# Kernel tuning notes

Hardware: AMD Instinct MI355X
Metric: run time of the kernel (lower is better)

Reference implementation:

```python
import jax, jax.numpy as jnp
import numpy as np

B, NPG, C, DEG, DE = 64, 1024, 512, 32, 16  # graphs, nodes/graph, feat dim, avg degree, edge-feat dim
N = B * NPG
E = N * DEG
RATIO = 0.5


def setup_inputs() -> dict:
    key = jax.random.key(0)
    k1, k2, k3, k4 = jax.random.split(key, 4)
    x = jax.random.normal(k1, (N, C), dtype=jnp.float32)
    # edges drawn within each graph block so batch structure is respected
    local = jax.random.randint(k2, (2, E), 0, NPG, dtype=jnp.int32)
    offsets = jnp.repeat(jnp.arange(B, dtype=jnp.int32) * NPG, NPG * DEG)
    edge_index = local + offsets[None, :]
    edge_attr = jax.random.normal(k3, (E, DE), dtype=jnp.float32)
    batch = jnp.repeat(jnp.arange(B, dtype=jnp.int32), NPG)
    W = jax.random.normal(k4, (C, 1), dtype=jnp.float32) * (1.0 / np.sqrt(C))
    b = jnp.zeros((1,), dtype=jnp.float32)
    return {"x": x, "edge_index": edge_index, "edge_attr": edge_attr, "batch": batch,
            "W": W, "b": b, "num_graphs": B, "nodes_per_graph": NPG}


def _gcn_score(x, edge_index, W, b):
    # PyG GCNConv(in_channels, 1): add self-loops, symmetric D^-1/2 (A+I) D^-1/2 norm
    n = x.shape[0]
    loop = jnp.arange(n, dtype=edge_index.dtype)
    s = jnp.concatenate([edge_index[0], loop])
    d = jnp.concatenate([edge_index[1], loop])
    deg = jnp.zeros((n,), x.dtype).at[d].add(jnp.ones((), x.dtype))  # >= 1 via self loops
    dinv = jax.lax.rsqrt(deg)
    norm = dinv[s] * dinv[d]                       # [E+n]
    h = (x @ W)[:, 0]                               # project first: [n]
    score = jnp.zeros((n,), x.dtype).at[d].add(h[s] * norm) + b[0]
    return score


def reference(x, edge_index, edge_attr, batch, W, b, num_graphs, nodes_per_graph):
    n = x.shape[0]
    k = int(np.ceil(RATIO * nodes_per_graph))
    score = _gcn_score(x, edge_index, W, b)         # [n]
    # per-graph top-k (equal-sized graphs -> fixed-shape top_k over [B, NPG])
    sc = score.reshape(num_graphs, nodes_per_graph)
    _, topi = jax.lax.top_k(sc, k)                  # [B, k], score-descending per graph
    offs = (jnp.arange(num_graphs, dtype=edge_index.dtype) * nodes_per_graph)[:, None]
    perm = (topi.astype(edge_index.dtype) + offs).reshape(-1)  # [B*k]
    x_new = x[perm] * jnp.tanh(score[perm])[:, None]
    batch_new = batch[perm]
    # filter_adj: keep edges with both endpoints selected, remap to new ids.
    # Fixed-shape version: full-length edge list with invalid entries = -1 plus a mask.
    sel = jnp.zeros((n,), bool).at[perm].set(True)
    newidx = jnp.full((n,), -1, edge_index.dtype).at[perm].set(
        jnp.arange(perm.shape[0], dtype=edge_index.dtype))
    src, dst = edge_index[0], edge_index[1]
    edge_mask = sel[src] & sel[dst]                 # [E]
    ei_new = jnp.where(edge_mask[None, :], jnp.stack([newidx[src], newidx[dst]]), -1)
    ea_new = jnp.where(edge_mask[:, None], edge_attr, jnp.zeros((), edge_attr.dtype))
    return x_new, ei_new, ea_new, edge_mask, batch_new, perm
```

## Files before the change

kernel.cpp:

```cpp
#include <hip/hip_runtime.h>
#include <math.h>

#define N_NODES 65536
#define C_DIM   512
#define E_EDGES 2097152
#define DE_DIM  16
#define B_GR    64
#define NPG     1024
#define DEG     32
#define EPG     (NPG * DEG)
#define K_SEL   512
#define NK      (B_GR * K_SEL)

#define OUT_XNEW  0
#define OUT_EI    (NK * C_DIM)
#define OUT_EA    (OUT_EI + 2 * E_EDGES)
#define OUT_MASK  (OUT_EA + (size_t)E_EDGES * DE_DIM)
#define OUT_BATCH (OUT_MASK + E_EDGES)
#define OUT_PERM  (OUT_BATCH + NK)

#define HIST_BLKS B_GR

__global__ void k_front(const float* __restrict__ x,
                        const float* __restrict__ W,
                        const int* __restrict__ dst,
                        float* __restrict__ h,
                        float* __restrict__ di) {
    __shared__ int   cnt[NPG];
    __shared__ float sW[C_DIM];

    if (blockIdx.x < HIST_BLKS) {
        const int g = blockIdx.x, t = threadIdx.x;
#pragma unroll
        for (int i = 0; i < 4; ++i) cnt[t + 256 * i] = 0;
        __syncthreads();

        const int4* dv = (const int4*)(dst + (size_t)g * EPG);
#pragma unroll
        for (int i = 0; i < 32; ++i) {
            int4 a = dv[t + 256 * i];
            atomicAdd(&cnt[a.x & (NPG - 1)], 1);
            atomicAdd(&cnt[a.y & (NPG - 1)], 1);
            atomicAdd(&cnt[a.z & (NPG - 1)], 1);
            atomicAdd(&cnt[a.w & (NPG - 1)], 1);
        }
        __syncthreads();

#pragma unroll
        for (int i = 0; i < 4; ++i) {
            const int n = t + 256 * i;
            di[(size_t)g * NPG + n] = rsqrtf((float)cnt[n] + 1.0f);
        }
    } else {
        const int t = threadIdx.x;
        ((float2*)sW)[t] = ((const float2*)W)[t];
        __syncthreads();

        const int wave = t >> 6, lane = t & 63;
        const int node = (blockIdx.x - HIST_BLKS) * 4 + wave;
        const float* xr = x + (size_t)node * C_DIM + lane * 8;
        float4 a0 = ((const float4*)xr)[0];
        float4 a1 = ((const float4*)xr)[1];
        const float* wr = sW + lane * 8;
        float s = a0.x * wr[0] + a0.y * wr[1] + a0.z * wr[2] + a0.w * wr[3]
                + a1.x * wr[4] + a1.y * wr[5] + a1.z * wr[6] + a1.w * wr[7];
#pragma unroll
        for (int off = 32; off > 0; off >>= 1) s += __shfl_down(s, off, 64);
        if (lane == 0) h[node] = s;
    }
}

__global__ void __launch_bounds__(1024)
k_select(const int* __restrict__ src, const int* __restrict__ dst,
         const float* __restrict__ h, const float* __restrict__ di,
         const float* __restrict__ b,
         int*   __restrict__ newidx, int* __restrict__ permw,
         float* __restrict__ mult,
         float* __restrict__ out_perm, float* __restrict__ out_batch) {
    __shared__ float hd[NPG];
    __shared__ float scp[NPG];
    __shared__ float scs[NPG];
    __shared__ unsigned long long keys[NPG];

    const int g = blockIdx.x, t = threadIdx.x;
    const int nbase = g * NPG;

    const float di_t = di[nbase + t];
    hd[t]  = h[nbase + t] * di_t;
    scp[t] = 0.0f;
    __syncthreads();

    const int4* sv = (const int4*)(src + (size_t)g * EPG);
    const int4* dv = (const int4*)(dst + (size_t)g * EPG);
#pragma unroll
    for (int i = 0; i < 8; ++i) {
        int4 sa = sv[t + NPG * i];
        int4 da = dv[t + NPG * i];
        unsafeAtomicAdd(&scp[da.x & (NPG - 1)], hd[sa.x & (NPG - 1)]);
        unsafeAtomicAdd(&scp[da.y & (NPG - 1)], hd[sa.y & (NPG - 1)]);
        unsafeAtomicAdd(&scp[da.z & (NPG - 1)], hd[sa.z & (NPG - 1)]);
        unsafeAtomicAdd(&scp[da.w & (NPG - 1)], hd[sa.w & (NPG - 1)]);
    }
    __syncthreads();

    {
        const float scf = (scp[t] + hd[t]) * di_t + b[0];
        scs[t] = scf;
        const unsigned int bits = __float_as_uint(scf);
        const unsigned int u = bits ^ ((bits & 0x80000000u) ? 0xFFFFFFFFu : 0x80000000u);
        keys[t] = ((unsigned long long)(~u) << 32) | (unsigned int)t;
    }
    __syncthreads();

    for (int k = 2; k <= NPG; k <<= 1) {
        for (int j = k >> 1; j > 0; j >>= 1) {
            if (t < NPG / 2) {
                const int i = ((t & ~(j - 1)) << 1) | (t & (j - 1));
                const int p = i | j;
                const bool asc = (i & k) == 0;
                const unsigned long long a = keys[i], bb = keys[p];
                if ((a > bb) == asc) { keys[i] = bb; keys[p] = a; }
            }
            __syncthreads();
        }
    }

    const int li   = (int)(keys[t] & 0xFFFFFFFFull);
    const int node = nbase + li;
    if (t < K_SEL) {
        const int j  = g * K_SEL + t;
        permw[j]     = node;
        newidx[node] = j;
        mult[j]      = tanhf(scs[li]);
        out_perm[j]  = (float)node;
        out_batch[j] = (float)g;
    } else {
        newidx[node] = -1;
    }
}

#define EDGE_BLKS (E_EDGES / 64)
#define XNEW_BLKS (NK / 2)

__global__ void k_tail(const float* __restrict__ x,
                       const float* __restrict__ mult,
                       const int* __restrict__ permw,
                       const int* __restrict__ src,
                       const int* __restrict__ dst,
                       const float* __restrict__ ea,
                       const int* __restrict__ newidx,
                       float* __restrict__ out_xnew,
                       float* __restrict__ out_ei,
                       float* __restrict__ out_ea,
                       float* __restrict__ out_mask) {
    int bid = blockIdx.x;
    if (bid < EDGE_BLKS) {
        const int gid = bid * 256 + threadIdx.x;
        const int e = gid >> 2, c = gid & 3;
        const int s = src[e], d = dst[e];
        const int ns = newidx[s], nd = newidx[d];
        const bool m = (ns >= 0) && (nd >= 0);

        float4 v = make_float4(0.f, 0.f, 0.f, 0.f);
        if (m) v = ((const float4*)ea)[(size_t)e * 4 + c];
        ((float4*)out_ea)[(size_t)e * 4 + c] = v;

        if (c == 0) {
            out_ei[e]           = m ? (float)ns : -1.0f;
            out_ei[E_EDGES + e] = m ? (float)nd : -1.0f;
            out_mask[e]         = m ? 1.0f : 0.0f;
        }
    } else {
        bid -= EDGE_BLKS;
        const int row = bid * 2 + (threadIdx.x >> 7);
        const int c   = (threadIdx.x & 127) * 4;
        const int node = permw[row];
        const float tt = mult[row];
        float4 v = *(const float4*)(x + (size_t)node * C_DIM + c);
        v.x *= tt; v.y *= tt; v.z *= tt; v.w *= tt;
        *(float4*)(out_xnew + (size_t)row * C_DIM + c) = v;
    }
}

extern "C" void kernel_launch(void* const* d_in, const int* in_sizes, int n_in,
                              void* d_out, int out_size, void* d_ws, size_t ws_size,
                              hipStream_t stream) {
    const float* x  = (const float*)d_in[0];
    const int*   ei = (const int*)d_in[1];
    const float* ea = (const float*)d_in[2];
    const float* W  = (const float*)d_in[4];
    const float* b  = (const float*)d_in[5];
    const int* src = ei;
    const int* dst = ei + E_EDGES;

    float* out = (float*)d_out;

    float* h      = (float*)d_ws;
    float* di     = h + N_NODES;
    float* mult   = di + N_NODES;
    int*   permw  = (int*)(mult + NK);
    int*   newidx = permw + NK;

    k_front<<<HIST_BLKS + N_NODES / 4, 256, 0, stream>>>(x, W, dst, h, di);
    k_select<<<B_GR, 1024, 0, stream>>>(src, dst, h, di, b,
                                        newidx, permw, mult,
                                        out + OUT_PERM, out + OUT_BATCH);
    k_tail<<<EDGE_BLKS + XNEW_BLKS, 256, 0, stream>>>(x, mult, permw, src, dst, ea,
                                                      newidx, out + OUT_XNEW,
                                                      out + OUT_EI, out + OUT_EA,
                                                      out + OUT_MASK);
}
```

Measured before the change: 481.6 us.

## Split score scatter across blocks, register bitonic sort, nontemporal tail accesses

The per-graph edge scatter moves into a separate kernel that splits each graph's edges over four blocks and merges partial sums with global atomics, so 256 blocks run instead of 64. Top-k becomes a register-resident bitonic sort that uses wave shuffles for strides below 64 and shared memory only for larger strides, which halves idle threads and cuts barriers. The streaming loads and stores in the tail kernel become nontemporal to avoid polluting the cache. The cost is an extra launch, global float atomics that make the summation order nondeterministic, and a score buffer that has to be zeroed.

```diff
diff --git a/kernel.cpp b/kernel.cpp
--- a/kernel.cpp
+++ b/kernel.cpp
@@ -9,8 +9,12 @@
 #define NPG     1024
 #define DEG     32
 #define EPG     (NPG * DEG)
+#define PARTS   4
+#define EPP     (EPG / PARTS)
 #define K_SEL   512
 #define NK      (B_GR * K_SEL)
+
+typedef float f32x4 __attribute__((ext_vector_type(4)));
 
 #define OUT_XNEW  0
 #define OUT_EI    (NK * C_DIM)
@@ -25,7 +29,8 @@
                         const float* __restrict__ W,
                         const int* __restrict__ dst,
                         float* __restrict__ h,
-                        float* __restrict__ di) {
+                        float* __restrict__ di,
+                        float* __restrict__ score) {
     __shared__ int   cnt[NPG];
     __shared__ float sW[C_DIM];
 
@@ -49,7 +54,8 @@
 #pragma unroll
         for (int i = 0; i < 4; ++i) {
             const int n = t + 256 * i;
-            di[(size_t)g * NPG + n] = rsqrtf((float)cnt[n] + 1.0f);
+            di[(size_t)g * NPG + n]    = rsqrtf((float)cnt[n] + 1.0f);
+            score[(size_t)g * NPG + n] = 0.0f;
         }
     } else {
         const int t = threadIdx.x;
@@ -71,61 +77,79 @@
 }
 
 __global__ void __launch_bounds__(1024)
-k_select(const int* __restrict__ src, const int* __restrict__ dst,
-         const float* __restrict__ h, const float* __restrict__ di,
-         const float* __restrict__ b,
-         int*   __restrict__ newidx, int* __restrict__ permw,
-         float* __restrict__ mult,
-         float* __restrict__ out_perm, float* __restrict__ out_batch) {
+k_score(const int* __restrict__ src, const int* __restrict__ dst,
+        const float* __restrict__ h, const float* __restrict__ di,
+        float* __restrict__ score) {
     __shared__ float hd[NPG];
     __shared__ float scp[NPG];
+    const int bg = blockIdx.x;
+    const int g = bg >> 2, part = bg & 3;
+    const int t = threadIdx.x;
+    const int nbase = g * NPG;
+
+    hd[t]  = h[nbase + t] * di[nbase + t];
+    scp[t] = 0.0f;
+    __syncthreads();
+
+    const int4* sv = (const int4*)(src + (size_t)g * EPG + part * EPP);
+    const int4* dv = (const int4*)(dst + (size_t)g * EPG + part * EPP);
+    int4 sa = sv[t], sb = sv[1024 + t];
+    int4 da = dv[t], db = dv[1024 + t];
+    unsafeAtomicAdd(&scp[da.x & (NPG - 1)], hd[sa.x & (NPG - 1)]);
+    unsafeAtomicAdd(&scp[da.y & (NPG - 1)], hd[sa.y & (NPG - 1)]);
+    unsafeAtomicAdd(&scp[da.z & (NPG - 1)], hd[sa.z & (NPG - 1)]);
+    unsafeAtomicAdd(&scp[da.w & (NPG - 1)], hd[sa.w & (NPG - 1)]);
+    unsafeAtomicAdd(&scp[db.x & (NPG - 1)], hd[sb.x & (NPG - 1)]);
+    unsafeAtomicAdd(&scp[db.y & (NPG - 1)], hd[sb.y & (NPG - 1)]);
+    unsafeAtomicAdd(&scp[db.z & (NPG - 1)], hd[sb.z & (NPG - 1)]);
+    unsafeAtomicAdd(&scp[db.w & (NPG - 1)], hd[sb.w & (NPG - 1)]);
+    __syncthreads();
+
+    unsafeAtomicAdd(&score[nbase + t], scp[t]);
+}
+
+__global__ void __launch_bounds__(1024)
+k_topk(const float* __restrict__ score, const float* __restrict__ h,
+       const float* __restrict__ di, const float* __restrict__ b,
+       int*   __restrict__ newidx, int* __restrict__ permw,
+       float* __restrict__ mult,
+       float* __restrict__ out_perm, float* __restrict__ out_batch) {
     __shared__ float scs[NPG];
-    __shared__ unsigned long long keys[NPG];
-
+    __shared__ unsigned long long skey[NPG];
     const int g = blockIdx.x, t = threadIdx.x;
     const int nbase = g * NPG;
 
-    const float di_t = di[nbase + t];
-    hd[t]  = h[nbase + t] * di_t;
-    scp[t] = 0.0f;
-    __syncthreads();
-
-    const int4* sv = (const int4*)(src + (size_t)g * EPG);
-    const int4* dv = (const int4*)(dst + (size_t)g * EPG);
-#pragma unroll
-    for (int i = 0; i < 8; ++i) {
-        int4 sa = sv[t + NPG * i];
-        int4 da = dv[t + NPG * i];
-        unsafeAtomicAdd(&scp[da.x & (NPG - 1)], hd[sa.x & (NPG - 1)]);
-        unsafeAtomicAdd(&scp[da.y & (NPG - 1)], hd[sa.y & (NPG - 1)]);
-        unsafeAtomicAdd(&scp[da.z & (NPG - 1)], hd[sa.z & (NPG - 1)]);
-        unsafeAtomicAdd(&scp[da.w & (NPG - 1)], hd[sa.w & (NPG - 1)]);
-    }
-    __syncthreads();
-
+    unsigned long long key;
     {
-        const float scf = (scp[t] + hd[t]) * di_t + b[0];
+        const float di_t = di[nbase + t];
+        const float hdt  = h[nbase + t] * di_t;
+        const float scf  = (score[nbase + t] + hdt) * di_t + b[0];
         scs[t] = scf;
         const unsigned int bits = __float_as_uint(scf);
         const unsigned int u = bits ^ ((bits & 0x80000000u) ? 0xFFFFFFFFu : 0x80000000u);
-        keys[t] = ((unsigned long long)(~u) << 32) | (unsigned int)t;
-    }
-    __syncthreads();
+        key = ((unsigned long long)(~u) << 32) | (unsigned int)t;
+    }
 
     for (int k = 2; k <= NPG; k <<= 1) {
         for (int j = k >> 1; j > 0; j >>= 1) {
-            if (t < NPG / 2) {
-                const int i = ((t & ~(j - 1)) << 1) | (t & (j - 1));
-                const int p = i | j;
-                const bool asc = (i & k) == 0;
-                const unsigned long long a = keys[i], bb = keys[p];
-                if ((a > bb) == asc) { keys[i] = bb; keys[p] = a; }
+            unsigned long long other;
+            if (j >= 64) {
+                __syncthreads();
+                skey[t] = key;
+                __syncthreads();
+                other = skey[t ^ j];
+            } else {
+                other = __shfl_xor(key, j, 64);
             }
-            __syncthreads();
-        }
-    }
-
-    const int li   = (int)(keys[t] & 0xFFFFFFFFull);
+            const bool up      = ((t & k) == 0);
+            const bool lower   = ((t & j) == 0);
+            const bool keepmin = (up == lower);
+            key = keepmin ? (key < other ? key : other)
+                          : (key > other ? key : other);
+        }
+    }
+
+    const int li   = (int)(key & 0xFFFFFFFFull);
     const int node = nbase + li;
     if (t < K_SEL) {
         const int j  = g * K_SEL + t;
@@ -161,14 +185,14 @@
         const int ns = newidx[s], nd = newidx[d];
         const bool m = (ns >= 0) && (nd >= 0);
 
-        float4 v = make_float4(0.f, 0.f, 0.f, 0.f);
-        if (m) v = ((const float4*)ea)[(size_t)e * 4 + c];
-        ((float4*)out_ea)[(size_t)e * 4 + c] = v;
+        f32x4 v = (f32x4)(0.0f);
+        if (m) v = __builtin_nontemporal_load((const f32x4*)ea + (size_t)e * 4 + c);
+        __builtin_nontemporal_store(v, (f32x4*)out_ea + (size_t)e * 4 + c);
 
         if (c == 0) {
-            out_ei[e]           = m ? (float)ns : -1.0f;
-            out_ei[E_EDGES + e] = m ? (float)nd : -1.0f;
-            out_mask[e]         = m ? 1.0f : 0.0f;
+            __builtin_nontemporal_store(m ? (float)ns : -1.0f, out_ei + e);
+            __builtin_nontemporal_store(m ? (float)nd : -1.0f, out_ei + E_EDGES + e);
+            __builtin_nontemporal_store(m ? 1.0f : 0.0f,       out_mask + e);
         }
     } else {
         bid -= EDGE_BLKS;
@@ -176,9 +200,9 @@
         const int c   = (threadIdx.x & 127) * 4;
         const int node = permw[row];
         const float tt = mult[row];
-        float4 v = *(const float4*)(x + (size_t)node * C_DIM + c);
-        v.x *= tt; v.y *= tt; v.z *= tt; v.w *= tt;
-        *(float4*)(out_xnew + (size_t)row * C_DIM + c) = v;
+        f32x4 v = __builtin_nontemporal_load((const f32x4*)(x + (size_t)node * C_DIM + c));
+        v *= tt;
+        __builtin_nontemporal_store(v, (f32x4*)(out_xnew + (size_t)row * C_DIM + c));
     }
 }
 
@@ -197,14 +221,15 @@
 
     float* h      = (float*)d_ws;
     float* di     = h + N_NODES;
-    float* mult   = di + N_NODES;
+    float* score  = di + N_NODES;
+    float* mult   = score + N_NODES;
     int*   permw  = (int*)(mult + NK);
     int*   newidx = permw + NK;
 
-    k_front<<<HIST_BLKS + N_NODES / 4, 256, 0, stream>>>(x, W, dst, h, di);
-    k_select<<<B_GR, 1024, 0, stream>>>(src, dst, h, di, b,
-                                        newidx, permw, mult,
-                                        out + OUT_PERM, out + OUT_BATCH);
+    k_front<<<HIST_BLKS + N_NODES / 4, 256, 0, stream>>>(x, W, dst, h, di, score);
+    k_score<<<B_GR * PARTS, 1024, 0, stream>>>(src, dst, h, di, score);
+    k_topk<<<B_GR, 1024, 0, stream>>>(score, h, di, b, newidx, permw, mult,
+                                      out + OUT_PERM, out + OUT_BATCH);
     k_tail<<<EDGE_BLKS + XNEW_BLKS, 256, 0, stream>>>(x, mult, permw, src, dst, ea,
                                                       newidx, out + OUT_XNEW,
                                                       out + OUT_EI, out + OUT_EA,
```

Result: faster. 443.8 us (-7.8%).
